# Performance work log

Hardware: AMD Instinct MI355X
Metric: run time of the kernel (lower is better)

## Reference

```python
import jax, jax.numpy as jnp
import numpy as np


def setup_inputs() -> dict:
    key = jax.random.key(0)
    ks = jax.random.split(key, 5)
    B, S, D, H, E = 2, 2048, 1024, 2816, 8
    x = jax.random.normal(ks[0], (B, S, D), dtype=jnp.float32)
    Wg = jax.random.normal(ks[1], (E, D), dtype=jnp.float32) * 0.02
    W1 = jax.random.normal(ks[2], (E, H, D), dtype=jnp.float32) * 0.02
    W2 = jax.random.normal(ks[3], (E, H, D), dtype=jnp.float32) * 0.02
    W3 = jax.random.normal(ks[4], (E, D, H), dtype=jnp.float32) * 0.02
    return {"x": x, "Wg": Wg, "W1": W1, "W2": W2, "W3": W3}


TOP_K = 2


def reference(x, Wg, W1, W2, W3):
    B, S, D = x.shape
    E = Wg.shape[0]
    xt = x.reshape(B * S, D)  # [T, D]
    # gating: raw logits, NO softmax (matches original module)
    scores = xt @ Wg.T  # [T, E]
    topk_scores, topk_idx = jax.lax.top_k(scores, TOP_K)  # [T, K]
    # dense per-expert SwiGLU FFN over all tokens, combined with sparse weights
    gate = jax.nn.silu(jnp.einsum('td,ehd->teh', xt, W1))  # [T, E, H]
    up = jnp.einsum('td,ehd->teh', xt, W2)                 # [T, E, H]
    y = jnp.einsum('teh,edh->ted', gate * up, W3)           # [T, E, D]
    # combine weights: w[t, e] = sum_k topk_scores[t, k] * (topk_idx[t, k] == e)
    onehot = jax.nn.one_hot(topk_idx, E, dtype=x.dtype)     # [T, K, E]
    w = jnp.einsum('tke,tk->te', onehot, topk_scores)       # [T, E]
    out = jnp.einsum('te,ted->td', w, y)                    # [T, D]
    return out.reshape(B, S, D)
```

## Files before the change

### kernel.cpp

```cpp
#include <hip/hip_runtime.h>
#include <hip/hip_bf16.h>
#include <stdint.h>


#define T_TOK 4096
#define DDIM 1024
#define HDIM 2816
#define NEXP 8

typedef __attribute__((ext_vector_type(8))) short short8;
typedef __attribute__((ext_vector_type(4))) short short4v;
typedef __attribute__((ext_vector_type(4))) float floatx4;

__device__ __forceinline__ short f2bf(float f) {
  union { float f; unsigned int u; } v; v.f = f;
  unsigned int u = v.u;
  u += 0x7FFFu + ((u >> 16) & 1u);
  return (short)(u >> 16);
}

__device__ __forceinline__ void gl2lds16(const void* g, void* l) {
  __builtin_amdgcn_global_load_lds(
      (const __attribute__((address_space(1))) void*)g,
      (__attribute__((address_space(3))) void*)l, 16, 0, 0);
}

#define CONV_ELEM4 5767168
__global__ __launch_bounds__(256) void convert_kernel(
    const float* __restrict__ W1, const float* __restrict__ W2, const float* __restrict__ W3,
    short* __restrict__ W1bf, short* __restrict__ W2bf, short* __restrict__ W3bf) {
  int z = blockIdx.y;
  const float4* src = (const float4*)((z == 0) ? W1 : (z == 1) ? W2 : W3);
  short4v* dst = (short4v*)((z == 0) ? W1bf : (z == 1) ? W2bf : W3bf);
  size_t stride = (size_t)gridDim.x * 256;
  for (size_t i = (size_t)blockIdx.x * 256 + threadIdx.x; i < CONV_ELEM4; i += stride) {
    float4 v = src[i];
    dst[i] = (short4v){f2bf(v.x), f2bf(v.y), f2bf(v.z), f2bf(v.w)};
  }
}

__global__ __launch_bounds__(64) void gating_score_kernel(const float* __restrict__ x,
    const float* __restrict__ Wg, short* __restrict__ xbf,
    int* __restrict__ re, float* __restrict__ rw) {
  int t = blockIdx.x;
  int lane = threadIdx.x;
  const float* xt = x + (size_t)t * DDIM;
  float xr[16];
#pragma unroll
  for (int j = 0; j < 16; ++j) xr[j] = xt[j * 64 + lane];
  short* xbt = xbf + (size_t)t * DDIM;
#pragma unroll
  for (int j = 0; j < 16; ++j) xbt[j * 64 + lane] = f2bf(xr[j]);
  float s[NEXP];
#pragma unroll
  for (int e = 0; e < NEXP; ++e) {
    const float* wge = Wg + e * DDIM;
    float p = 0.f;
#pragma unroll
    for (int j = 0; j < 16; ++j) p += xr[j] * wge[j * 64 + lane];
#pragma unroll
    for (int o = 32; o > 0; o >>= 1) p += __shfl_xor(p, o, 64);
    s[e] = p;
  }
  if (lane == 0) {
    int e1 = 0; float s1 = s[0];
#pragma unroll
    for (int e = 1; e < NEXP; ++e) if (s[e] > s1) { s1 = s[e]; e1 = e; }
    int e2 = -1; float s2 = -1e30f;
#pragma unroll
    for (int e = 0; e < NEXP; ++e) if (e != e1 && s[e] > s2) { s2 = s[e]; e2 = e; }
    re[2 * t] = e1;     rw[2 * t] = s1;
    re[2 * t + 1] = e2; rw[2 * t + 1] = s2;
  }
}

__global__ __launch_bounds__(1024) void route_kernel(const int* __restrict__ re,
    int* __restrict__ counts, int* __restrict__ offs,
    int* __restrict__ rs, int* __restrict__ tlist) {
  __shared__ int H[NEXP * 1024];
  __shared__ int totS[NEXP];
  int tid = threadIdx.x;
  int myre[8];
  int cnt[NEXP];
#pragma unroll
  for (int e = 0; e < NEXP; ++e) cnt[e] = 0;
  const int4* re4 = (const int4*)(re + tid * 8);
  int4 a = re4[0], b = re4[1];
  myre[0] = a.x; myre[1] = a.y; myre[2] = a.z; myre[3] = a.w;
  myre[4] = b.x; myre[5] = b.y; myre[6] = b.z; myre[7] = b.w;
#pragma unroll
  for (int j = 0; j < 8; ++j) cnt[myre[j]]++;
#pragma unroll
  for (int e = 0; e < NEXP; ++e) H[e * 1024 + tid] = cnt[e];
  __syncthreads();
  int wave = tid >> 6, lane = tid & 63;
  if (wave < NEXP) {
    int run = 0;
    for (int c = 0; c < 16; ++c) {
      int i = c * 64 + lane;
      int v = H[wave * 1024 + i];
      int sc = v;
#pragma unroll
      for (int o = 1; o < 64; o <<= 1) {
        int u = __shfl_up(sc, o, 64);
        if (lane >= o) sc += u;
      }
      int tot = __shfl(sc, 63, 64);
      H[wave * 1024 + i] = run + sc - v;
      run += tot;
    }
    if (lane == 0) totS[wave] = run;
  }
  __syncthreads();
  if (tid == 0) {
    int run = 0;
    for (int e = 0; e < NEXP; ++e) {
      offs[e] = run; counts[e] = totS[e]; run += totS[e];
    }
  }
  int pos[NEXP];
#pragma unroll
  for (int e = 0; e < NEXP; ++e) pos[e] = H[e * 1024 + tid];
#pragma unroll
  for (int j = 0; j < 8; ++j) {
    int e = myre[j];
    int slot = pos[e]++;
    int idx = tid * 8 + j;
    rs[idx] = slot;
    tlist[e * T_TOK + slot] = idx >> 1;
  }
}

__global__ __launch_bounds__(256) void ffn1_fast_kernel(const short* __restrict__ xbf,
    const short* __restrict__ W1bf, const short* __restrict__ W2bf,
    const int* __restrict__ counts, const int* __restrict__ offs,
    const int* __restrict__ tlist, short* __restrict__ hmat) {
  int e = blockIdx.z;
  int cnt = counts[e];
  int m0 = blockIdx.y * 128;
  if (m0 >= cnt) return;
  int n0 = blockIdx.x * 64;
  __shared__ __attribute__((aligned(16))) short As[128 * 32];
  __shared__ __attribute__((aligned(16))) short Bs1[64 * 32];
  __shared__ __attribute__((aligned(16))) short Bs2[64 * 32];
  __shared__ int toks[128];
  int tid = threadIdx.x;
  if (tid < 128) {
    int m = m0 + tid;
    toks[tid] = tlist[e * T_TOK + (m < cnt ? m : cnt - 1)];
  }
  __syncthreads();
  int lane = tid & 63, w = tid >> 6;
  int wr = w >> 1, wc = w & 1;
  int lrow = lane & 15, lq = lane >> 4;
  int lr = lane >> 2;
  int lc = (lane & 3) * 8;
  const short* pA0 = xbf + (size_t)toks[w * 32 + lr] * DDIM + lc;
  const short* pA1 = xbf + (size_t)toks[w * 32 + 16 + lr] * DDIM + lc;
  const short* b1e = W1bf + (size_t)e * HDIM * DDIM;
  const short* b2e = W2bf + (size_t)e * HDIM * DDIM;
  const short* pB1 = b1e + (size_t)(n0 + w * 16 + lr) * DDIM + lc;
  const short* pB2 = b2e + (size_t)(n0 + w * 16 + lr) * DDIM + lc;
  void* lA0 = (void*)&As[(2 * w) * 512];
  void* lA1 = (void*)&As[(2 * w + 1) * 512];
  void* lB1 = (void*)&Bs1[w * 512];
  void* lB2 = (void*)&Bs2[w * 512];
  floatx4 accg[4][2], accu[4][2];
#pragma unroll
  for (int i = 0; i < 4; ++i)
#pragma unroll
    for (int j = 0; j < 2; ++j) {
      accg[i][j] = (floatx4){0.f, 0.f, 0.f, 0.f};
      accu[i][j] = (floatx4){0.f, 0.f, 0.f, 0.f};
    }
  for (int kk = 0; kk < DDIM; kk += 32) {
    gl2lds16(pA0, lA0);
    gl2lds16(pA1, lA1);
    gl2lds16(pB1, lB1);
    gl2lds16(pB2, lB2);
    pA0 += 32; pA1 += 32; pB1 += 32; pB2 += 32;
    __syncthreads();
    short8 a[4], b1[2], b2[2];
#pragma unroll
    for (int mf = 0; mf < 4; ++mf)
      a[mf] = *(short8*)&As[(wr * 64 + mf * 16 + lrow) * 32 + lq * 8];
#pragma unroll
    for (int nf = 0; nf < 2; ++nf) {
      b1[nf] = *(short8*)&Bs1[(wc * 32 + nf * 16 + lrow) * 32 + lq * 8];
      b2[nf] = *(short8*)&Bs2[(wc * 32 + nf * 16 + lrow) * 32 + lq * 8];
    }
#pragma unroll
    for (int mf = 0; mf < 4; ++mf)
#pragma unroll
      for (int nf = 0; nf < 2; ++nf) {
        accg[mf][nf] = __builtin_amdgcn_mfma_f32_16x16x32_bf16(a[mf], b1[nf], accg[mf][nf], 0, 0, 0);
        accu[mf][nf] = __builtin_amdgcn_mfma_f32_16x16x32_bf16(a[mf], b2[nf], accu[mf][nf], 0, 0, 0);
      }
    __syncthreads();
  }
  int base = offs[e];
#pragma unroll
  for (int mf = 0; mf < 4; ++mf)
#pragma unroll
    for (int r = 0; r < 4; ++r) {
      int mloc = wr * 64 + mf * 16 + lq * 4 + r;
      if (m0 + mloc < cnt) {
        size_t row = (size_t)(base + m0 + mloc);
#pragma unroll
        for (int nf = 0; nf < 2; ++nf) {
          float g = accg[mf][nf][r];
          float u = accu[mf][nf][r];
          float h = g / (1.f + __expf(-g)) * u;
          hmat[row * HDIM + n0 + wc * 32 + nf * 16 + lrow] = f2bf(h);
        }
      }
    }
}

#define KSPLIT 2
#define KHALF (HDIM / KSPLIT)
__global__ __launch_bounds__(256) void ffn2_fast_kernel(const short* __restrict__ hmat,
    const short* __restrict__ W3bf,
    const int* __restrict__ counts, const int* __restrict__ offs,
    float* __restrict__ ypart0, float* __restrict__ ypart1) {
  int e = blockIdx.z;
  int cnt = counts[e];
  int m0 = blockIdx.y * 128;
  if (m0 >= cnt) return;
  int ks = blockIdx.x >> 3;
  int n0 = (blockIdx.x & 7) * 128;
  int k0 = ks * KHALF;
  float* ypart = ks ? ypart1 : ypart0;
  int base = offs[e];
  __shared__ __attribute__((aligned(16))) short As[128 * 32];
  __shared__ __attribute__((aligned(16))) short Bs[128 * 32];
  int tid = threadIdx.x;
  int lane = tid & 63, w = tid >> 6;
  int wr = w >> 1, wc = w & 1;
  int lrow = lane & 15, lq = lane >> 4;
  int lr = lane >> 2;
  int lc = (lane & 3) * 8;
  int gA0 = m0 + w * 32 + lr;      gA0 = gA0 < cnt ? gA0 : cnt - 1;
  int gA1 = m0 + w * 32 + 16 + lr; gA1 = gA1 < cnt ? gA1 : cnt - 1;
  const short* pA0 = hmat + (size_t)(base + gA0) * HDIM + k0 + lc;
  const short* pA1 = hmat + (size_t)(base + gA1) * HDIM + k0 + lc;
  const short* W3e = W3bf + (size_t)e * DDIM * HDIM;
  const short* pB0 = W3e + (size_t)(n0 + w * 32 + lr) * HDIM + k0 + lc;
  const short* pB1 = W3e + (size_t)(n0 + w * 32 + 16 + lr) * HDIM + k0 + lc;
  void* lA0 = (void*)&As[(2 * w) * 512];
  void* lA1 = (void*)&As[(2 * w + 1) * 512];
  void* lB0 = (void*)&Bs[(2 * w) * 512];
  void* lB1 = (void*)&Bs[(2 * w + 1) * 512];
  floatx4 acc[4][4];
#pragma unroll
  for (int i = 0; i < 4; ++i)
#pragma unroll
    for (int j = 0; j < 4; ++j) acc[i][j] = (floatx4){0.f, 0.f, 0.f, 0.f};
  for (int kk = 0; kk < KHALF; kk += 32) {
    gl2lds16(pA0, lA0);
    gl2lds16(pA1, lA1);
    gl2lds16(pB0, lB0);
    gl2lds16(pB1, lB1);
    pA0 += 32; pA1 += 32; pB0 += 32; pB1 += 32;
    __syncthreads();
    short8 a[4], b[4];
#pragma unroll
    for (int mf = 0; mf < 4; ++mf)
      a[mf] = *(short8*)&As[(wr * 64 + mf * 16 + lrow) * 32 + lq * 8];
#pragma unroll
    for (int nf = 0; nf < 4; ++nf)
      b[nf] = *(short8*)&Bs[(wc * 64 + nf * 16 + lrow) * 32 + lq * 8];
#pragma unroll
    for (int mf = 0; mf < 4; ++mf)
#pragma unroll
      for (int nf = 0; nf < 4; ++nf)
        acc[mf][nf] = __builtin_amdgcn_mfma_f32_16x16x32_bf16(a[mf], b[nf], acc[mf][nf], 0, 0, 0);
    __syncthreads();
  }
#pragma unroll
  for (int mf = 0; mf < 4; ++mf)
#pragma unroll
    for (int r = 0; r < 4; ++r) {
      int mloc = wr * 64 + mf * 16 + lq * 4 + r;
      if (m0 + mloc < cnt) {
        float* orow = ypart + (size_t)(base + m0 + mloc) * DDIM + n0 + wc * 64 + lrow;
#pragma unroll
        for (int nf = 0; nf < 4; ++nf)
          orow[nf * 16] = acc[mf][nf][r];
      }
    }
}

__global__ __launch_bounds__(256) void combine_kernel(const float4* __restrict__ y0,
    const float4* __restrict__ y1,
    const int* __restrict__ offs, const int* __restrict__ re, const int* __restrict__ rs,
    const float* __restrict__ rw, float4* __restrict__ out4) {
  int t = blockIdx.x;
  int i = threadIdx.x;
  size_t r0 = (size_t)(offs[re[2 * t]] + rs[2 * t]) * 256 + i;
  size_t r1 = (size_t)(offs[re[2 * t + 1]] + rs[2 * t + 1]) * 256 + i;
  float w0 = rw[2 * t], w1 = rw[2 * t + 1];
  float4 a0 = y0[r0], a1 = y1[r0];
  float4 b0 = y0[r1], b1 = y1[r1];
  out4[(size_t)t * 256 + i] = make_float4(
      w0 * (a0.x + a1.x) + w1 * (b0.x + b1.x),
      w0 * (a0.y + a1.y) + w1 * (b0.y + b1.y),
      w0 * (a0.z + a1.z) + w1 * (b0.z + b1.z),
      w0 * (a0.w + a1.w) + w1 * (b0.w + b1.w));
}

extern "C" void kernel_launch(void* const* d_in, const int* in_sizes, int n_in,
                              void* d_out, int out_size, void* d_ws, size_t ws_size,
                              hipStream_t stream) {
  const float* x  = (const float*)d_in[0];
  const float* Wg = (const float*)d_in[1];
  const float* W1 = (const float*)d_in[2];
  const float* W2 = (const float*)d_in[3];
  const float* W3 = (const float*)d_in[4];
  float* out = (float*)d_out;
  char* ws = (char*)d_ws;

  int*   counts = (int*)(ws + 0);
  int*   offs   = (int*)(ws + 256);
  int*   tlist  = (int*)(ws + 512);
  int*   re     = (int*)(ws + 131584);
  int*   rs     = (int*)(ws + 164352);
  float* rw     = (float*)(ws + 197120);
  short* xbf    = (short*)(ws + 229888);
  short* hmat   = (short*)(ws + 8618496);
  short* W3bf   = (short*)(ws + 54755840);
  short* W1bf   = (short*)(ws + 100893184);
  short* W2bf   = (short*)(ws + 147030528);
  float* ypart0 = (float*)(ws + 100893184);
  float* ypart1 = (float*)(ws + 147030528);

  convert_kernel<<<dim3(4096, 3), 256, 0, stream>>>(W1, W2, W3, W1bf, W2bf, W3bf);
  gating_score_kernel<<<T_TOK, 64, 0, stream>>>(x, Wg, xbf, re, rw);
  route_kernel<<<1, 1024, 0, stream>>>(re, counts, offs, rs, tlist);
  ffn1_fast_kernel<<<dim3(HDIM / 64, T_TOK / 128, NEXP), 256, 0, stream>>>(
      xbf, W1bf, W2bf, counts, offs, tlist, hmat);
  ffn2_fast_kernel<<<dim3((DDIM / 128) * KSPLIT, T_TOK / 128, NEXP), 256, 0, stream>>>(
      hmat, W3bf, counts, offs, ypart0, ypart1);
  combine_kernel<<<T_TOK, 256, 0, stream>>>((const float4*)ypart0, (const float4*)ypart1,
                                            offs, re, rs, rw, (float4*)out);
}
```

Before: 539.9 us.

## Double K-tile depth to 64 with XOR-swizzled LDS layout in expert GEMMs

Both expert GEMM kernels now stage 64-wide K slices instead of 32 per barrier pair, halving the number of sync points and loop iterations. Global-to-LDS loads use an XOR swizzle on 16-byte column chunks, and the fragment reads apply the matching swizzle to avoid LDS bank conflicts with the wider row stride. The gating kernel packs four tokens per 256-thread block to cut block launch overhead. LDS use per block roughly doubles, which may reduce occupancy.

```diff
diff --git a/kernel.cpp b/kernel.cpp
--- a/kernel.cpp
+++ b/kernel.cpp
@@ -39,11 +39,11 @@
   }
 }
 
-__global__ __launch_bounds__(64) void gating_score_kernel(const float* __restrict__ x,
+__global__ __launch_bounds__(256) void gating_score_kernel(const float* __restrict__ x,
     const float* __restrict__ Wg, short* __restrict__ xbf,
     int* __restrict__ re, float* __restrict__ rw) {
-  int t = blockIdx.x;
-  int lane = threadIdx.x;
+  int t = blockIdx.x * 4 + (threadIdx.x >> 6);
+  int lane = threadIdx.x & 63;
   const float* xt = x + (size_t)t * DDIM;
   float xr[16];
 #pragma unroll
@@ -140,9 +140,9 @@
   int m0 = blockIdx.y * 128;
   if (m0 >= cnt) return;
   int n0 = blockIdx.x * 64;
-  __shared__ __attribute__((aligned(16))) short As[128 * 32];
-  __shared__ __attribute__((aligned(16))) short Bs1[64 * 32];
-  __shared__ __attribute__((aligned(16))) short Bs2[64 * 32];
+  __shared__ __attribute__((aligned(16))) short As[128 * 64];
+  __shared__ __attribute__((aligned(16))) short Bs1[64 * 64];
+  __shared__ __attribute__((aligned(16))) short Bs2[64 * 64];
   __shared__ int toks[128];
   int tid = threadIdx.x;
   if (tid < 128) {
@@ -153,18 +153,30 @@
   int lane = tid & 63, w = tid >> 6;
   int wr = w >> 1, wc = w & 1;
   int lrow = lane & 15, lq = lane >> 4;
-  int lr = lane >> 2;
-  int lc = (lane & 3) * 8;
-  const short* pA0 = xbf + (size_t)toks[w * 32 + lr] * DDIM + lc;
-  const short* pA1 = xbf + (size_t)toks[w * 32 + 16 + lr] * DDIM + lc;
+  int sr = lane >> 3;
+  int sc = lane & 7;
+  int scs = ((sc ^ sr) & 7) * 8;
+  const short* pA[4];
+#pragma unroll
+  for (int j = 0; j < 4; ++j)
+    pA[j] = xbf + (size_t)toks[w * 32 + j * 8 + sr] * DDIM + scs;
   const short* b1e = W1bf + (size_t)e * HDIM * DDIM;
   const short* b2e = W2bf + (size_t)e * HDIM * DDIM;
-  const short* pB1 = b1e + (size_t)(n0 + w * 16 + lr) * DDIM + lc;
-  const short* pB2 = b2e + (size_t)(n0 + w * 16 + lr) * DDIM + lc;
-  void* lA0 = (void*)&As[(2 * w) * 512];
-  void* lA1 = (void*)&As[(2 * w + 1) * 512];
-  void* lB1 = (void*)&Bs1[w * 512];
-  void* lB2 = (void*)&Bs2[w * 512];
+  const short* pB1[2]; const short* pB2[2];
+#pragma unroll
+  for (int j = 0; j < 2; ++j) {
+    int row = w * 16 + j * 8 + sr;
+    pB1[j] = b1e + (size_t)(n0 + row) * DDIM + scs;
+    pB2[j] = b2e + (size_t)(n0 + row) * DDIM + scs;
+  }
+  void* lA[4]; void* lB1[2]; void* lB2[2];
+#pragma unroll
+  for (int j = 0; j < 4; ++j) lA[j] = (void*)&As[(w * 32 + j * 8) * 64];
+#pragma unroll
+  for (int j = 0; j < 2; ++j) {
+    lB1[j] = (void*)&Bs1[(w * 16 + j * 8) * 64];
+    lB2[j] = (void*)&Bs2[(w * 16 + j * 8) * 64];
+  }
   floatx4 accg[4][2], accu[4][2];
 #pragma unroll
   for (int i = 0; i < 4; ++i)
@@ -173,29 +185,35 @@
       accg[i][j] = (floatx4){0.f, 0.f, 0.f, 0.f};
       accu[i][j] = (floatx4){0.f, 0.f, 0.f, 0.f};
     }
-  for (int kk = 0; kk < DDIM; kk += 32) {
-    gl2lds16(pA0, lA0);
-    gl2lds16(pA1, lA1);
-    gl2lds16(pB1, lB1);
-    gl2lds16(pB2, lB2);
-    pA0 += 32; pA1 += 32; pB1 += 32; pB2 += 32;
+  for (int kk = 0; kk < DDIM; kk += 64) {
+#pragma unroll
+    for (int j = 0; j < 4; ++j) { gl2lds16(pA[j], lA[j]); pA[j] += 64; }
+#pragma unroll
+    for (int j = 0; j < 2; ++j) {
+      gl2lds16(pB1[j], lB1[j]); pB1[j] += 64;
+      gl2lds16(pB2[j], lB2[j]); pB2[j] += 64;
+    }
     __syncthreads();
-    short8 a[4], b1[2], b2[2];
-#pragma unroll
-    for (int mf = 0; mf < 4; ++mf)
-      a[mf] = *(short8*)&As[(wr * 64 + mf * 16 + lrow) * 32 + lq * 8];
-#pragma unroll
-    for (int nf = 0; nf < 2; ++nf) {
-      b1[nf] = *(short8*)&Bs1[(wc * 32 + nf * 16 + lrow) * 32 + lq * 8];
-      b2[nf] = *(short8*)&Bs2[(wc * 32 + nf * 16 + lrow) * 32 + lq * 8];
-    }
-#pragma unroll
-    for (int mf = 0; mf < 4; ++mf)
+#pragma unroll
+    for (int kh = 0; kh < 2; ++kh) {
+      int csw = (((kh * 4 + lq) ^ (lrow & 7)) & 7) * 8;
+      short8 a[4], b1[2], b2[2];
+#pragma unroll
+      for (int mf = 0; mf < 4; ++mf)
+        a[mf] = *(short8*)&As[(wr * 64 + mf * 16 + lrow) * 64 + csw];
 #pragma unroll
       for (int nf = 0; nf < 2; ++nf) {
-        accg[mf][nf] = __builtin_amdgcn_mfma_f32_16x16x32_bf16(a[mf], b1[nf], accg[mf][nf], 0, 0, 0);
-        accu[mf][nf] = __builtin_amdgcn_mfma_f32_16x16x32_bf16(a[mf], b2[nf], accu[mf][nf], 0, 0, 0);
+        b1[nf] = *(short8*)&Bs1[(wc * 32 + nf * 16 + lrow) * 64 + csw];
+        b2[nf] = *(short8*)&Bs2[(wc * 32 + nf * 16 + lrow) * 64 + csw];
       }
+#pragma unroll
+      for (int mf = 0; mf < 4; ++mf)
+#pragma unroll
+        for (int nf = 0; nf < 2; ++nf) {
+          accg[mf][nf] = __builtin_amdgcn_mfma_f32_16x16x32_bf16(a[mf], b1[nf], accg[mf][nf], 0, 0, 0);
+          accu[mf][nf] = __builtin_amdgcn_mfma_f32_16x16x32_bf16(a[mf], b2[nf], accu[mf][nf], 0, 0, 0);
+        }
+    }
     __syncthreads();
   }
   int base = offs[e];
@@ -232,49 +250,54 @@
   int k0 = ks * KHALF;
   float* ypart = ks ? ypart1 : ypart0;
   int base = offs[e];
-  __shared__ __attribute__((aligned(16))) short As[128 * 32];
-  __shared__ __attribute__((aligned(16))) short Bs[128 * 32];
+  __shared__ __attribute__((aligned(16))) short As[128 * 64];
+  __shared__ __attribute__((aligned(16))) short Bs[128 * 64];
   int tid = threadIdx.x;
   int lane = tid & 63, w = tid >> 6;
   int wr = w >> 1, wc = w & 1;
   int lrow = lane & 15, lq = lane >> 4;
-  int lr = lane >> 2;
-  int lc = (lane & 3) * 8;
-  int gA0 = m0 + w * 32 + lr;      gA0 = gA0 < cnt ? gA0 : cnt - 1;
-  int gA1 = m0 + w * 32 + 16 + lr; gA1 = gA1 < cnt ? gA1 : cnt - 1;
-  const short* pA0 = hmat + (size_t)(base + gA0) * HDIM + k0 + lc;
-  const short* pA1 = hmat + (size_t)(base + gA1) * HDIM + k0 + lc;
+  int sr = lane >> 3;
+  int sc = lane & 7;
+  int scs = ((sc ^ sr) & 7) * 8;
   const short* W3e = W3bf + (size_t)e * DDIM * HDIM;
-  const short* pB0 = W3e + (size_t)(n0 + w * 32 + lr) * HDIM + k0 + lc;
-  const short* pB1 = W3e + (size_t)(n0 + w * 32 + 16 + lr) * HDIM + k0 + lc;
-  void* lA0 = (void*)&As[(2 * w) * 512];
-  void* lA1 = (void*)&As[(2 * w + 1) * 512];
-  void* lB0 = (void*)&Bs[(2 * w) * 512];
-  void* lB1 = (void*)&Bs[(2 * w + 1) * 512];
+  const short* pA[4]; const short* pB[4];
+  void* lA[4]; void* lB[4];
+#pragma unroll
+  for (int j = 0; j < 4; ++j) {
+    int gr = m0 + w * 32 + j * 8 + sr;
+    gr = gr < cnt ? gr : cnt - 1;
+    pA[j] = hmat + (size_t)(base + gr) * HDIM + k0 + scs;
+    pB[j] = W3e + (size_t)(n0 + w * 32 + j * 8 + sr) * HDIM + k0 + scs;
+    lA[j] = (void*)&As[(w * 32 + j * 8) * 64];
+    lB[j] = (void*)&Bs[(w * 32 + j * 8) * 64];
+  }
   floatx4 acc[4][4];
 #pragma unroll
   for (int i = 0; i < 4; ++i)
 #pragma unroll
     for (int j = 0; j < 4; ++j) acc[i][j] = (floatx4){0.f, 0.f, 0.f, 0.f};
-  for (int kk = 0; kk < KHALF; kk += 32) {
-    gl2lds16(pA0, lA0);
-    gl2lds16(pA1, lA1);
-    gl2lds16(pB0, lB0);
-    gl2lds16(pB1, lB1);
-    pA0 += 32; pA1 += 32; pB0 += 32; pB1 += 32;
+  for (int kk = 0; kk < KHALF; kk += 64) {
+#pragma unroll
+    for (int j = 0; j < 4; ++j) { gl2lds16(pA[j], lA[j]); pA[j] += 64; }
+#pragma unroll
+    for (int j = 0; j < 4; ++j) { gl2lds16(pB[j], lB[j]); pB[j] += 64; }
     __syncthreads();
-    short8 a[4], b[4];
-#pragma unroll
-    for (int mf = 0; mf < 4; ++mf)
-      a[mf] = *(short8*)&As[(wr * 64 + mf * 16 + lrow) * 32 + lq * 8];
-#pragma unroll
-    for (int nf = 0; nf < 4; ++nf)
-      b[nf] = *(short8*)&Bs[(wc * 64 + nf * 16 + lrow) * 32 + lq * 8];
-#pragma unroll
-    for (int mf = 0; mf < 4; ++mf)
+#pragma unroll
+    for (int kh = 0; kh < 2; ++kh) {
+      int csw = (((kh * 4 + lq) ^ (lrow & 7)) & 7) * 8;
+      short8 a[4], b[4];
+#pragma unroll
+      for (int mf = 0; mf < 4; ++mf)
+        a[mf] = *(short8*)&As[(wr * 64 + mf * 16 + lrow) * 64 + csw];
 #pragma unroll
       for (int nf = 0; nf < 4; ++nf)
-        acc[mf][nf] = __builtin_amdgcn_mfma_f32_16x16x32_bf16(a[mf], b[nf], acc[mf][nf], 0, 0, 0);
+        b[nf] = *(short8*)&Bs[(wc * 64 + nf * 16 + lrow) * 64 + csw];
+#pragma unroll
+      for (int mf = 0; mf < 4; ++mf)
+#pragma unroll
+        for (int nf = 0; nf < 4; ++nf)
+          acc[mf][nf] = __builtin_amdgcn_mfma_f32_16x16x32_bf16(a[mf], b[nf], acc[mf][nf], 0, 0, 0);
+    }
     __syncthreads();
   }
 #pragma unroll
@@ -335,7 +358,7 @@
   float* ypart1 = (float*)(ws + 147030528);
 
   convert_kernel<<<dim3(4096, 3), 256, 0, stream>>>(W1, W2, W3, W1bf, W2bf, W3bf);
-  gating_score_kernel<<<T_TOK, 64, 0, stream>>>(x, Wg, xbf, re, rw);
+  gating_score_kernel<<<T_TOK / 4, 256, 0, stream>>>(x, Wg, xbf, re, rw);
   route_kernel<<<1, 1024, 0, stream>>>(re, counts, offs, rs, tlist);
   ffn1_fast_kernel<<<dim3(HDIM / 64, T_TOK / 128, NEXP), 256, 0, stream>>>(
       xbf, W1bf, W2bf, counts, offs, tlist, hmat);
```

After: 528.6 us. 1.02x faster.
